# Optimization experiments

Measured on AMD Instinct MI355X. Metric: run time of the kernel, lower is better.

Reference implementation:

```python
import jax, jax.numpy as jnp
import numpy as np

TEMPERATURE = 0.04
LAMBDA_KOLEO = 0.1
EPS_NORM = 1e-12
EPS_KOLEO = 1e-9


def setup_inputs() -> dict:
    key = jax.random.key(0)
    k1, k2 = jax.random.split(key)
    N, D = 8192, 512
    z1 = jax.random.normal(k1, (N, D), dtype=jnp.float32)
    z2 = jax.random.normal(k2, (N, D), dtype=jnp.float32)
    return {"z1": z1, "z2": z2}


def _l2_normalize(x):
    # matches F.normalize(x, dim=1) with default eps=1e-12
    n = jnp.linalg.norm(x, axis=1, keepdims=True)
    return x / jnp.maximum(n, EPS_NORM)


def _infonce(queries, keys, temperature):
    # [N, N] similarity logits; labels are the diagonal
    logits = (queries @ keys.T) / temperature
    logp = jax.nn.log_softmax(logits, axis=1)
    return -jnp.mean(jnp.diagonal(logp))


def _koleo(emb):
    # pairwise euclidean distances via gram trick (matches torch.cdist p=2)
    sq = jnp.sum(emb * emb, axis=1)
    d2 = sq[:, None] + sq[None, :] - 2.0 * (emb @ emb.T)
    d = jnp.sqrt(jnp.maximum(d2, 0.0))
    N = emb.shape[0]
    eye = jnp.eye(N, dtype=bool)
    d = jnp.where(eye, jnp.inf, d)
    min_d = jnp.min(d, axis=1)
    return -jnp.mean(jnp.log(min_d + EPS_KOLEO))


def reference(z1, z2):
    z1 = _l2_normalize(z1)
    z2 = _l2_normalize(z2)
    loss_12 = _infonce(z1, z2, TEMPERATURE)
    loss_21 = _infonce(z2, z1, TEMPERATURE)
    loss_contrastive = (loss_12 + loss_21) / 2
    koleo_1 = _koleo(z1)
    koleo_2 = _koleo(z2)
    loss_koleo = (koleo_1 + koleo_2) / 2
    total_loss = loss_contrastive + LAMBDA_KOLEO * loss_koleo
    return total_loss
```

## Files before the change

kernel.cpp:

```cpp
#include <hip/hip_runtime.h>
#include <hip/hip_bf16.h>
#include <hip/hip_fp8.h>
#include <math.h>

#define N 8192
#define D 512
#define BM 128
#define BK 64
#define NSTRIP 64
#define S_BLOCKS (NSTRIP * NSTRIP)
#define TRI (NSTRIP * (NSTRIP + 1) / 2)
#define G_BLOCKS (2 * TRI)
#define SG_BLOCKS (S_BLOCKS + G_BLOCKS)

typedef float f32x16 __attribute__((ext_vector_type(16)));
typedef int i32x4 __attribute__((ext_vector_type(4)));
typedef int i32x8 __attribute__((ext_vector_type(8)));

__device__ inline void gload_lds16(const void* g, void* l) {
  __builtin_amdgcn_global_load_lds(
      (const __attribute__((address_space(1))) void*)g,
      (__attribute__((address_space(3))) void*)l, 16, 0, 0);
}

__global__ __launch_bounds__(256) void norm_kernel(
    const float* __restrict__ z1, const float* __restrict__ z2,
    unsigned char* __restrict__ q1, unsigned char* __restrict__ q2,
    float* __restrict__ diag, float* __restrict__ out) {
  int t = threadIdx.x;
  int lane = t & 63;
  int w = t >> 6;
  int row = blockIdx.x * 4 + w;
  if (blockIdx.x == 0 && t == 0) out[0] = 0.0f;
  const float4* a = (const float4*)(z1 + (size_t)row * D);
  const float4* b = (const float4*)(z2 + (size_t)row * D);
  float4 xa0 = a[lane], xa1 = a[lane + 64];
  float4 xb0 = b[lane], xb1 = b[lane + 64];
  float ss1 = xa0.x * xa0.x + xa0.y * xa0.y + xa0.z * xa0.z + xa0.w * xa0.w +
              xa1.x * xa1.x + xa1.y * xa1.y + xa1.z * xa1.z + xa1.w * xa1.w;
  float ss2 = xb0.x * xb0.x + xb0.y * xb0.y + xb0.z * xb0.z + xb0.w * xb0.w +
              xb1.x * xb1.x + xb1.y * xb1.y + xb1.z * xb1.z + xb1.w * xb1.w;
  float dd = xa0.x * xb0.x + xa0.y * xb0.y + xa0.z * xb0.z + xa0.w * xb0.w +
             xa1.x * xb1.x + xa1.y * xb1.y + xa1.z * xb1.z + xa1.w * xb1.w;
#pragma unroll
  for (int off = 1; off < 64; off <<= 1) {
    ss1 += __shfl_xor(ss1, off);
    ss2 += __shfl_xor(ss2, off);
    dd  += __shfl_xor(dd,  off);
  }
  float i1 = 1.0f / fmaxf(sqrtf(ss1), 1e-12f);
  float i2 = 1.0f / fmaxf(sqrtf(ss2), 1e-12f);
  float fa[8] = {xa0.x, xa0.y, xa0.z, xa0.w, xa1.x, xa1.y, xa1.z, xa1.w};
  float fb[8] = {xb0.x, xb0.y, xb0.z, xb0.w, xb1.x, xb1.y, xb1.z, xb1.w};
  unsigned int u1[2], u2[2];
#pragma unroll
  for (int g = 0; g < 2; g++) {
    unsigned int v1 = 0, v2 = 0;
#pragma unroll
    for (int e = 0; e < 4; e++) {
      __hip_fp8_e4m3 c1(fa[g * 4 + e] * i1);
      __hip_fp8_e4m3 c2(fb[g * 4 + e] * i2);
      v1 |= ((unsigned int)c1.__x) << (8 * e);
      v2 |= ((unsigned int)c2.__x) << (8 * e);
    }
    u1[g] = v1; u2[g] = v2;
  }
  ((unsigned int*)q1)[(size_t)row * 128 + lane] = u1[0];
  ((unsigned int*)q1)[(size_t)row * 128 + 64 + lane] = u1[1];
  ((unsigned int*)q2)[(size_t)row * 128 + lane] = u2[0];
  ((unsigned int*)q2)[(size_t)row * 128 + 64 + lane] = u2[1];
  if (lane == 0) diag[row] = dd * i1 * i2;
}

__device__ __forceinline__ void stage_pair(
    const unsigned char* pA, const unsigned char* pB,
    unsigned char (*Ab)[BM * BK], unsigned char (*Bb)[BM * BK],
    int ldst, int chunk) {
  int buf = chunk & 3;
  int k0 = chunk * BK;
  gload_lds16(pA + k0, &Ab[buf][ldst]);
  gload_lds16(pA + 64 * D + k0, &Ab[buf][4096 + ldst]);
  gload_lds16(pB + k0, &Bb[buf][ldst]);
  gload_lds16(pB + 64 * D + k0, &Bb[buf][4096 + ldst]);
}

#define SG_ROUND(p, VM)                                                        \
  {                                                                            \
    asm volatile("s_waitcnt vmcnt(" #VM ")" ::: "memory");                     \
    __builtin_amdgcn_s_barrier();                                              \
    __builtin_amdgcn_sched_barrier(0);                                         \
    if ((p) < 5) stage_pair(pA, pB, Ab, Bb, ldst, (p) + 3);                    \
    const unsigned char* Ac = Ab[(p) & 3];                                     \
    const unsigned char* Bc = Bb[(p) & 3];                                     \
    i32x8 af[2], bf[2];                                                        \
    _Pragma("unroll")                                                          \
    for (int i = 0; i < 2; i++) {                                              \
      i32x4 lo = *(const i32x4*)(Ac + offA[i][0]);                             \
      i32x4 hi = *(const i32x4*)(Ac + offA[i][1]);                             \
      af[i] = __builtin_shufflevector(lo, hi, 0, 1, 2, 3, 4, 5, 6, 7);         \
      lo = *(const i32x4*)(Bc + offB[i][0]);                                   \
      hi = *(const i32x4*)(Bc + offB[i][1]);                                   \
      bf[i] = __builtin_shufflevector(lo, hi, 0, 1, 2, 3, 4, 5, 6, 7);         \
    }                                                                          \
    asm volatile("s_waitcnt lgkmcnt(0)" ::: "memory");                         \
    __builtin_amdgcn_sched_barrier(0);                                         \
    __builtin_amdgcn_s_setprio(1);                                             \
    _Pragma("unroll")                                                          \
    for (int i = 0; i < 2; i++)                                                \
      _Pragma("unroll")                                                        \
      for (int j = 0; j < 2; j++)                                              \
        acc[i][j] = __builtin_amdgcn_mfma_scale_f32_32x32x64_f8f6f4(           \
            af[i], bf[j], acc[i][j], 0, 0, 0, 0x7F7F7F7F, 0, 0x7F7F7F7F);      \
    __builtin_amdgcn_s_setprio(0);                                             \
    __builtin_amdgcn_sched_barrier(0);                                         \
  }

__device__ __forceinline__ void mm_tile_mx(
    const unsigned char* __restrict__ X, const unsigned char* __restrict__ Y,
    int r0, int c0, unsigned char (*Ab)[BM * BK], unsigned char (*Bb)[BM * BK],
    f32x16 (&acc)[2][2], int t, int l31, int h, int rw, int cw) {
#pragma unroll
  for (int i = 0; i < 2; i++)
#pragma unroll
    for (int j = 0; j < 2; j++)
#pragma unroll
      for (int r = 0; r < 16; r++) acc[i][j][r] = 0.0f;

  int srow = t >> 2;
  int ssrc = (t & 3) ^ ((t >> 3) & 3);
  const unsigned char* pA = X + (size_t)(r0 + srow) * D + ssrc * 16;
  const unsigned char* pB = Y + (size_t)(c0 + srow) * D + ssrc * 16;
  int ldst = t * 16;

  int offA[2][2], offB[2][2];
#pragma unroll
  for (int i = 0; i < 2; i++) {
    int row = rw * 64 + i * 32 + l31;
    int sw = (row >> 1) & 3;
    offA[i][0] = row * 64 + (((h << 1) | 0) ^ sw) * 16;
    offA[i][1] = row * 64 + (((h << 1) | 1) ^ sw) * 16;
  }
#pragma unroll
  for (int j = 0; j < 2; j++) {
    int row = cw * 64 + j * 32 + l31;
    int sw = (row >> 1) & 3;
    offB[j][0] = row * 64 + (((h << 1) | 0) ^ sw) * 16;
    offB[j][1] = row * 64 + (((h << 1) | 1) ^ sw) * 16;
  }

  stage_pair(pA, pB, Ab, Bb, ldst, 0);
  stage_pair(pA, pB, Ab, Bb, ldst, 1);
  stage_pair(pA, pB, Ab, Bb, ldst, 2);

  SG_ROUND(0, 8) SG_ROUND(1, 8) SG_ROUND(2, 8) SG_ROUND(3, 8)
  SG_ROUND(4, 8) SG_ROUND(5, 8) SG_ROUND(6, 4) SG_ROUND(7, 0)
}

__global__ __launch_bounds__(256, 2) void sg_kernel(
    const unsigned char* __restrict__ q1, const unsigned char* __restrict__ q2,
    float* __restrict__ rowS, float* __restrict__ colS,
    float* __restrict__ partG) {
  __shared__ unsigned char Ab[4][BM * BK];
  __shared__ unsigned char Bb[4][BM * BK];
  float (*redA)[BM] = reinterpret_cast<float (*)[BM]>(&Ab[0][0]);
  float (*redB)[BM] = reinterpret_cast<float (*)[BM]>(&Ab[0][0] + 1024);

  int bx = blockIdx.x;
  int t = threadIdx.x;
  int lane = t & 63;
  int wave = t >> 6;
  int l31 = lane & 31;
  int h = lane >> 5;
  int rw = wave >> 1;
  int cw = wave & 1;
  const float scale = 1.4426950408889634f / 0.04f;

  bool smode = bx < S_BLOCKS;
  const unsigned char* X;
  const unsigned char* Y;
  int r0, c0, ga = 0, gb = 0, gg = 0;
  bool diagb = false;
  if (smode) {
    r0 = (bx >> 6) * BM;
    c0 = (bx & 63) * BM;
    X = q1; Y = q2;
  } else {
    int gx = bx - S_BLOCKS;
    gg = (gx >= TRI) ? 1 : 0;
    int tri = gx - gg * TRI;
    int a = (int)((sqrtf(8.0f * (float)tri + 1.0f) - 1.0f) * 0.5f);
    while ((a + 1) * (a + 2) / 2 <= tri) a++;
    while (a * (a + 1) / 2 > tri) a--;
    int b = tri - a * (a + 1) / 2;
    ga = a; gb = b;
    X = gg ? q2 : q1; Y = X;
    r0 = a * BM;
    c0 = b * BM;
    diagb = (a == b);
  }

  f32x16 acc[2][2];
  mm_tile_mx(X, Y, r0, c0, Ab, Bb, acc, t, l31, h, rw, cw);

  __syncthreads();

  if (smode) {
    float csum[2] = {0.0f, 0.0f};
#pragma unroll
    for (int i = 0; i < 2; i++) {
      float rsum[16];
#pragma unroll
      for (int reg = 0; reg < 16; reg++) rsum[reg] = 0.0f;
#pragma unroll
      for (int j = 0; j < 2; j++)
#pragma unroll
        for (int reg = 0; reg < 16; reg++) {
          float e = __builtin_amdgcn_exp2f(acc[i][j][reg] * scale);
          rsum[reg] += e;
          csum[j] += e;
        }
#pragma unroll
      for (int reg = 0; reg < 16; reg++) {
#pragma unroll
        for (int off = 1; off < 32; off <<= 1) rsum[reg] += __shfl_xor(rsum[reg], off);
      }
      if (l31 == 0) {
#pragma unroll
        for (int reg = 0; reg < 16; reg++) {
          int rloc = (reg & 3) + 8 * (reg >> 2) + 4 * h;
          redB[cw][rw * 64 + i * 32 + rloc] = rsum[reg];
        }
      }
    }
#pragma unroll
    for (int j = 0; j < 2; j++) {
      csum[j] += __shfl_xor(csum[j], 32);
      if (h == 0) redA[rw][cw * 64 + j * 32 + l31] = csum[j];
    }
    __syncthreads();
    if (t < BM) {
      colS[(size_t)(r0 >> 7) * N + c0 + t] = redA[0][t] + redA[1][t];
      rowS[(size_t)(c0 >> 7) * N + r0 + t] = redB[0][t] + redB[1][t];
    }
  } else {
#pragma unroll
    for (int i = 0; i < 2; i++) {
      float rmax[16];
#pragma unroll
      for (int reg = 0; reg < 16; reg++) {
        int rloc = (reg & 3) + 8 * (reg >> 2) + 4 * h;
        int rr = rw * 64 + i * 32 + rloc;
        float v = -3.0e38f;
#pragma unroll
        for (int j = 0; j < 2; j++) {
          float x = acc[i][j][reg];
          int cc = cw * 64 + j * 32 + l31;
          if (diagb && cc == rr) x = -3.0e38f;
          v = fmaxf(v, x);
        }
        rmax[reg] = v;
      }
#pragma unroll
      for (int reg = 0; reg < 16; reg++) {
#pragma unroll
        for (int off = 1; off < 32; off <<= 1) rmax[reg] = fmaxf(rmax[reg], __shfl_xor(rmax[reg], off));
      }
      if (l31 == 0) {
#pragma unroll
        for (int reg = 0; reg < 16; reg++) {
          int rloc = (reg & 3) + 8 * (reg >> 2) + 4 * h;
          redA[cw][rw * 64 + i * 32 + rloc] = rmax[reg];
        }
      }
    }
    if (!diagb) {
#pragma unroll
      for (int j = 0; j < 2; j++) {
        float m = -3.0e38f;
#pragma unroll
        for (int i = 0; i < 2; i++)
#pragma unroll
          for (int reg = 0; reg < 16; reg++) m = fmaxf(m, acc[i][j][reg]);
        m = fmaxf(m, __shfl_xor(m, 32));
        if (h == 0) redB[rw][cw * 64 + j * 32 + l31] = m;
      }
    }
    __syncthreads();
    if (t < BM) {
      partG[((size_t)(gg * NSTRIP + gb)) * N + r0 + t] = fmaxf(redA[0][t], redA[1][t]);
      if (!diagb)
        partG[((size_t)(gg * NSTRIP + ga)) * N + c0 + t] = fmaxf(redB[0][t], redB[1][t]);
    }
  }
}

__global__ __launch_bounds__(256) void combine_kernel(
    const float* __restrict__ diag,
    const float* __restrict__ rowS, const float* __restrict__ colS,
    const float* __restrict__ partG, float* __restrict__ out) {
  int t = threadIdx.x;
  int l = t & 63;
  int w = t >> 6;
  int i = blockIdx.x * 64 + l;

  float sR = 0.0f, sC = 0.0f, g1 = -3.0e38f, g2 = -3.0e38f;
#pragma unroll
  for (int s = 0; s < 16; s++) {
    int strip = w * 16 + s;
    sR += rowS[(size_t)strip * N + i];
    sC += colS[(size_t)strip * N + i];
    g1 = fmaxf(g1, partG[(size_t)strip * N + i]);
    g2 = fmaxf(g2, partG[(size_t)(NSTRIP + strip) * N + i]);
  }
  __shared__ float red[4][4][64];
  red[0][w][l] = sR; red[1][w][l] = sC; red[2][w][l] = g1; red[3][w][l] = g2;
  __syncthreads();
  if (w == 0) {
    sR = red[0][0][l] + red[0][1][l] + red[0][2][l] + red[0][3][l];
    sC = red[1][0][l] + red[1][1][l] + red[1][2][l] + red[1][3][l];
    g1 = fmaxf(fmaxf(red[2][0][l], red[2][1][l]), fmaxf(red[2][2][l], red[2][3][l]));
    g2 = fmaxf(fmaxf(red[3][0][l], red[3][1][l]), fmaxf(red[3][2][l], red[3][3][l]));
    float dv = diag[i] * 25.0f;
    float a12 = logf(sR) - dv;
    float a21 = logf(sC) - dv;
    float k1 = logf(sqrtf(fmaxf(2.0f - 2.0f * g1, 0.0f)) + 1e-9f);
    float k2 = logf(sqrtf(fmaxf(2.0f - 2.0f * g2, 0.0f)) + 1e-9f);
    float c = 0.5f * (a12 + a21) / (float)N - 0.1f * 0.5f * (k1 + k2) / (float)N;
#pragma unroll
    for (int off = 1; off < 64; off <<= 1) c += __shfl_xor(c, off);
    if (l == 0) atomicAdd(out, c);
  }
}

extern "C" void kernel_launch(void* const* d_in, const int* in_sizes, int n_in,
                              void* d_out, int out_size, void* d_ws, size_t ws_size,
                              hipStream_t stream) {
  const float* z1 = (const float*)d_in[0];
  const float* z2 = (const float*)d_in[1];
  char* w = (char*)d_ws;
  unsigned char* q1 = (unsigned char*)w; w += (size_t)N * D;
  unsigned char* q2 = (unsigned char*)w; w += (size_t)N * D;
  float* diag = (float*)w;   w += (size_t)N * sizeof(float);
  float* rowS = (float*)w;   w += (size_t)NSTRIP * N * sizeof(float);
  float* colS = (float*)w;   w += (size_t)NSTRIP * N * sizeof(float);
  float* partG = (float*)w;  w += (size_t)2 * NSTRIP * N * sizeof(float);
  float* out = (float*)d_out;

  norm_kernel<<<N / 4, 256, 0, stream>>>(z1, z2, q1, q2, diag, out);
  sg_kernel<<<SG_BLOCKS, 256, 0, stream>>>(q1, q2, rowS, colS, partG);
  combine_kernel<<<N / 64, 256, 0, stream>>>(diag, rowS, colS, partG, out);
}
```

Measured before the change: 233.5 us.

## Enlarge similarity GEMM tiles to 256x256 with 8 waves and XCD-aware block mapping

Doubles the output tile of the fused FP8 similarity/Gram kernel from 128 to 256 rows and columns. Each block now runs 512 threads, each wave computing a 128x64 sub-tile, with a 128KB dynamic LDS four-stage buffer. Block indices are remapped so that blocks sharing bx&7 (likely the same XCD) work on neighbouring tiles, which should improve L2 reuse. The goal is higher arithmetic intensity and fewer global loads, at the cost of more registers, more LDS, lower occupancy, and a coarser tail.

```diff
diff --git a/kernel.cpp b/kernel.cpp
--- a/kernel.cpp
+++ b/kernel.cpp
@@ -5,13 +5,13 @@
 
 #define N 8192
 #define D 512
-#define BM 128
+#define BM 256
 #define BK 64
-#define NSTRIP 64
+#define NSTRIP 32
 #define S_BLOCKS (NSTRIP * NSTRIP)
-#define TRI (NSTRIP * (NSTRIP + 1) / 2)
-#define G_BLOCKS (2 * TRI)
+#define G_BLOCKS 1056
 #define SG_BLOCKS (S_BLOCKS + G_BLOCKS)
+#define QPX 260
 
 typedef float f32x16 __attribute__((ext_vector_type(16)));
 typedef int i32x4 __attribute__((ext_vector_type(4)));
@@ -72,16 +72,15 @@
   if (lane == 0) diag[row] = dd * i1 * i2;
 }
 
-__device__ __forceinline__ void stage_pair(
+__device__ __forceinline__ void stage_chunk(
     const unsigned char* pA, const unsigned char* pB,
-    unsigned char (*Ab)[BM * BK], unsigned char (*Bb)[BM * BK],
-    int ldst, int chunk) {
-  int buf = chunk & 3;
+    unsigned char* ldsb, int t, int chunk) {
+  unsigned char* buf = ldsb + (chunk & 3) * 32768;
   int k0 = chunk * BK;
-  gload_lds16(pA + k0, &Ab[buf][ldst]);
-  gload_lds16(pA + 64 * D + k0, &Ab[buf][4096 + ldst]);
-  gload_lds16(pB + k0, &Bb[buf][ldst]);
-  gload_lds16(pB + 64 * D + k0, &Bb[buf][4096 + ldst]);
+  gload_lds16(pA + k0,           buf + t * 16);
+  gload_lds16(pA + 128 * D + k0, buf + 8192 + t * 16);
+  gload_lds16(pB + k0,           buf + 16384 + t * 16);
+  gload_lds16(pB + 128 * D + k0, buf + 24576 + t * 16);
 }
 
 #define SG_ROUND(p, VM)                                                        \
@@ -89,24 +88,26 @@
     asm volatile("s_waitcnt vmcnt(" #VM ")" ::: "memory");                     \
     __builtin_amdgcn_s_barrier();                                              \
     __builtin_amdgcn_sched_barrier(0);                                         \
-    if ((p) < 5) stage_pair(pA, pB, Ab, Bb, ldst, (p) + 3);                    \
-    const unsigned char* Ac = Ab[(p) & 3];                                     \
-    const unsigned char* Bc = Bb[(p) & 3];                                     \
-    i32x8 af[2], bf[2];                                                        \
+    if ((p) < 5) stage_chunk(pA, pB, lds, t, (p) + 3);                         \
+    const unsigned char* buf = lds + (((p) & 3) * 32768);                      \
+    i32x8 af[4], bf[2];                                                        \
     _Pragma("unroll")                                                          \
-    for (int i = 0; i < 2; i++) {                                              \
-      i32x4 lo = *(const i32x4*)(Ac + offA[i][0]);                             \
-      i32x4 hi = *(const i32x4*)(Ac + offA[i][1]);                             \
+    for (int i = 0; i < 4; i++) {                                              \
+      i32x4 lo = *(const i32x4*)(buf + offA[i][0]);                            \
+      i32x4 hi = *(const i32x4*)(buf + offA[i][1]);                            \
       af[i] = __builtin_shufflevector(lo, hi, 0, 1, 2, 3, 4, 5, 6, 7);         \
-      lo = *(const i32x4*)(Bc + offB[i][0]);                                   \
-      hi = *(const i32x4*)(Bc + offB[i][1]);                                   \
-      bf[i] = __builtin_shufflevector(lo, hi, 0, 1, 2, 3, 4, 5, 6, 7);         \
+    }                                                                          \
+    _Pragma("unroll")                                                          \
+    for (int j = 0; j < 2; j++) {                                              \
+      i32x4 lo = *(const i32x4*)(buf + 16384 + offB[j][0]);                    \
+      i32x4 hi = *(const i32x4*)(buf + 16384 + offB[j][1]);                    \
+      bf[j] = __builtin_shufflevector(lo, hi, 0, 1, 2, 3, 4, 5, 6, 7);         \
     }                                                                          \
     asm volatile("s_waitcnt lgkmcnt(0)" ::: "memory");                         \
     __builtin_amdgcn_sched_barrier(0);                                         \
     __builtin_amdgcn_s_setprio(1);                                             \
     _Pragma("unroll")                                                          \
-    for (int i = 0; i < 2; i++)                                                \
+    for (int i = 0; i < 4; i++)                                                \
       _Pragma("unroll")                                                        \
       for (int j = 0; j < 2; j++)                                              \
         acc[i][j] = __builtin_amdgcn_mfma_scale_f32_32x32x64_f8f6f4(           \
@@ -115,27 +116,71 @@
     __builtin_amdgcn_sched_barrier(0);                                         \
   }
 
-__device__ __forceinline__ void mm_tile_mx(
-    const unsigned char* __restrict__ X, const unsigned char* __restrict__ Y,
-    int r0, int c0, unsigned char (*Ab)[BM * BK], unsigned char (*Bb)[BM * BK],
-    f32x16 (&acc)[2][2], int t, int l31, int h, int rw, int cw) {
-#pragma unroll
-  for (int i = 0; i < 2; i++)
-#pragma unroll
-    for (int j = 0; j < 2; j++)
-#pragma unroll
-      for (int r = 0; r < 16; r++) acc[i][j][r] = 0.0f;
-
-  int srow = t >> 2;
-  int ssrc = (t & 3) ^ ((t >> 3) & 3);
-  const unsigned char* pA = X + (size_t)(r0 + srow) * D + ssrc * 16;
-  const unsigned char* pB = Y + (size_t)(c0 + srow) * D + ssrc * 16;
-  int ldst = t * 16;
-
-  int offA[2][2], offB[2][2];
-#pragma unroll
-  for (int i = 0; i < 2; i++) {
-    int row = rw * 64 + i * 32 + l31;
+__global__ __launch_bounds__(512, 2) void sg_kernel(
+    const unsigned char* __restrict__ q1, const unsigned char* __restrict__ q2,
+    float* __restrict__ rowS, float* __restrict__ colS,
+    float* __restrict__ partG) {
+  extern __shared__ unsigned char lds[];
+  float (*redR)[256] = (float (*)[256])lds;
+  float (*redC)[256] = (float (*)[256])(lds + 4096);
+
+  int bx = blockIdx.x;
+  int x = bx & 7;
+  int q = bx >> 3;
+  int t = threadIdx.x;
+  int lane = t & 63;
+  int wv = t >> 6;
+  int l31 = lane & 31;
+  int h = lane >> 5;
+  int rw = wv >> 2;
+  int cw = wv & 3;
+  const float scale = 1.4426950408889634f / 0.04f;
+
+  bool smode = q < 128;
+  const unsigned char* X;
+  const unsigned char* Y;
+  int r0, c0, ga = 0, gb = 0, gg = 0;
+  bool diagb = false;
+  if (smode) {
+    int u = x >> 1, v = x & 1;
+    int r = u * 8 + (q >> 4);
+    int c = v * 16 + (q & 15);
+    r0 = r * BM; c0 = c * BM;
+    X = q1; Y = q2;
+  } else {
+    int qq = q - 128;
+    int a4, b4, g;
+    if (qq < 20) {
+      g = qq / 10;
+      int tt = qq - g * 10;
+      int da = (int)((sqrtf(8.0f * (float)tt + 1.0f) - 1.0f) * 0.5f);
+      while ((da + 1) * (da + 2) / 2 <= tt) da++;
+      while (da * (da + 1) / 2 > tt) da--;
+      int db = tt - da * (da + 1) / 2;
+      a4 = x * 4 + da; b4 = x * 4 + db;
+    } else {
+      int e = qq - 20;
+      int n = e >> 4;
+      int tt = e & 15;
+      int pidx = x + 8 * n;
+      g = (pidx >= 28) ? 1 : 0;
+      int p = pidx - g * 28;
+      int i = (int)((sqrtf(8.0f * (float)p + 1.0f) + 1.0f) * 0.5f);
+      while (i * (i - 1) / 2 > p) i--;
+      while ((i + 1) * i / 2 <= p) i++;
+      int j = p - i * (i - 1) / 2;
+      a4 = i * 4 + (tt >> 2); b4 = j * 4 + (tt & 3);
+    }
+    ga = a4; gb = b4; gg = g;
+    X = g ? q2 : q1; Y = X;
+    r0 = a4 * BM; c0 = b4 * BM;
+    diagb = (a4 == b4);
+  }
+
+  int offA[4][2], offB[2][2];
+#pragma unroll
+  for (int i = 0; i < 4; i++) {
+    int row = rw * 128 + i * 32 + l31;
     int sw = (row >> 1) & 3;
     offA[i][0] = row * 64 + (((h << 1) | 0) ^ sw) * 16;
     offA[i][1] = row * 64 + (((h << 1) | 1) ^ sw) * 16;
@@ -148,128 +193,95 @@
     offB[j][1] = row * 64 + (((h << 1) | 1) ^ sw) * 16;
   }
 
-  stage_pair(pA, pB, Ab, Bb, ldst, 0);
-  stage_pair(pA, pB, Ab, Bb, ldst, 1);
-  stage_pair(pA, pB, Ab, Bb, ldst, 2);
+  int srow = t >> 2;
+  int ssrc = (t & 3) ^ ((t >> 3) & 3);
+  const unsigned char* pA = X + (size_t)(r0 + srow) * D + ssrc * 16;
+  const unsigned char* pB = Y + (size_t)(c0 + srow) * D + ssrc * 16;
+
+  f32x16 acc[4][2];
+#pragma unroll
+  for (int i = 0; i < 4; i++)
+#pragma unroll
+    for (int j = 0; j < 2; j++)
+#pragma unroll
+      for (int r = 0; r < 16; r++) acc[i][j][r] = 0.0f;
+
+  stage_chunk(pA, pB, lds, t, 0);
+  stage_chunk(pA, pB, lds, t, 1);
+  stage_chunk(pA, pB, lds, t, 2);
 
   SG_ROUND(0, 8) SG_ROUND(1, 8) SG_ROUND(2, 8) SG_ROUND(3, 8)
   SG_ROUND(4, 8) SG_ROUND(5, 8) SG_ROUND(6, 4) SG_ROUND(7, 0)
-}
-
-__global__ __launch_bounds__(256, 2) void sg_kernel(
-    const unsigned char* __restrict__ q1, const unsigned char* __restrict__ q2,
-    float* __restrict__ rowS, float* __restrict__ colS,
-    float* __restrict__ partG) {
-  __shared__ unsigned char Ab[4][BM * BK];
-  __shared__ unsigned char Bb[4][BM * BK];
-  float (*redA)[BM] = reinterpret_cast<float (*)[BM]>(&Ab[0][0]);
-  float (*redB)[BM] = reinterpret_cast<float (*)[BM]>(&Ab[0][0] + 1024);
-
-  int bx = blockIdx.x;
-  int t = threadIdx.x;
-  int lane = t & 63;
-  int wave = t >> 6;
-  int l31 = lane & 31;
-  int h = lane >> 5;
-  int rw = wave >> 1;
-  int cw = wave & 1;
-  const float scale = 1.4426950408889634f / 0.04f;
-
-  bool smode = bx < S_BLOCKS;
-  const unsigned char* X;
-  const unsigned char* Y;
-  int r0, c0, ga = 0, gb = 0, gg = 0;
-  bool diagb = false;
-  if (smode) {
-    r0 = (bx >> 6) * BM;
-    c0 = (bx & 63) * BM;
-    X = q1; Y = q2;
-  } else {
-    int gx = bx - S_BLOCKS;
-    gg = (gx >= TRI) ? 1 : 0;
-    int tri = gx - gg * TRI;
-    int a = (int)((sqrtf(8.0f * (float)tri + 1.0f) - 1.0f) * 0.5f);
-    while ((a + 1) * (a + 2) / 2 <= tri) a++;
-    while (a * (a + 1) / 2 > tri) a--;
-    int b = tri - a * (a + 1) / 2;
-    ga = a; gb = b;
-    X = gg ? q2 : q1; Y = X;
-    r0 = a * BM;
-    c0 = b * BM;
-    diagb = (a == b);
-  }
-
-  f32x16 acc[2][2];
-  mm_tile_mx(X, Y, r0, c0, Ab, Bb, acc, t, l31, h, rw, cw);
 
   __syncthreads();
 
   if (smode) {
     float csum[2] = {0.0f, 0.0f};
 #pragma unroll
-    for (int i = 0; i < 2; i++) {
+    for (int i = 0; i < 4; i++) {
       float rsum[16];
 #pragma unroll
-      for (int reg = 0; reg < 16; reg++) rsum[reg] = 0.0f;
+      for (int r = 0; r < 16; r++) rsum[r] = 0.0f;
 #pragma unroll
       for (int j = 0; j < 2; j++)
 #pragma unroll
-        for (int reg = 0; reg < 16; reg++) {
-          float e = __builtin_amdgcn_exp2f(acc[i][j][reg] * scale);
-          rsum[reg] += e;
+        for (int r = 0; r < 16; r++) {
+          float e = __builtin_amdgcn_exp2f(acc[i][j][r] * scale);
+          rsum[r] += e;
           csum[j] += e;
         }
 #pragma unroll
-      for (int reg = 0; reg < 16; reg++) {
-#pragma unroll
-        for (int off = 1; off < 32; off <<= 1) rsum[reg] += __shfl_xor(rsum[reg], off);
+      for (int r = 0; r < 16; r++) {
+#pragma unroll
+        for (int off = 1; off < 32; off <<= 1) rsum[r] += __shfl_xor(rsum[r], off);
       }
       if (l31 == 0) {
 #pragma unroll
-        for (int reg = 0; reg < 16; reg++) {
-          int rloc = (reg & 3) + 8 * (reg >> 2) + 4 * h;
-          redB[cw][rw * 64 + i * 32 + rloc] = rsum[reg];
+        for (int r = 0; r < 16; r++) {
+          int rloc = (r & 3) + 8 * (r >> 2) + 4 * h;
+          redR[cw][rw * 128 + i * 32 + rloc] = rsum[r];
         }
       }
     }
 #pragma unroll
     for (int j = 0; j < 2; j++) {
       csum[j] += __shfl_xor(csum[j], 32);
-      if (h == 0) redA[rw][cw * 64 + j * 32 + l31] = csum[j];
+      if (h == 0) redC[rw][cw * 64 + j * 32 + l31] = csum[j];
     }
     __syncthreads();
     if (t < BM) {
-      colS[(size_t)(r0 >> 7) * N + c0 + t] = redA[0][t] + redA[1][t];
-      rowS[(size_t)(c0 >> 7) * N + r0 + t] = redB[0][t] + redB[1][t];
+      rowS[(size_t)(c0 >> 8) * N + r0 + t] =
+          redR[0][t] + redR[1][t] + redR[2][t] + redR[3][t];
+      colS[(size_t)(r0 >> 8) * N + c0 + t] = redC[0][t] + redC[1][t];
     }
   } else {
 #pragma unroll
-    for (int i = 0; i < 2; i++) {
+    for (int i = 0; i < 4; i++) {
       float rmax[16];
 #pragma unroll
-      for (int reg = 0; reg < 16; reg++) {
-        int rloc = (reg & 3) + 8 * (reg >> 2) + 4 * h;
-        int rr = rw * 64 + i * 32 + rloc;
+      for (int r = 0; r < 16; r++) {
+        int rloc = (r & 3) + 8 * (r >> 2) + 4 * h;
+        int rr = rw * 128 + i * 32 + rloc;
         float v = -3.0e38f;
 #pragma unroll
         for (int j = 0; j < 2; j++) {
-          float x = acc[i][j][reg];
+          float xv = acc[i][j][r];
           int cc = cw * 64 + j * 32 + l31;
-          if (diagb && cc == rr) x = -3.0e38f;
-          v = fmaxf(v, x);
+          if (diagb && cc == rr) xv = -3.0e38f;
+          v = fmaxf(v, xv);
         }
-        rmax[reg] = v;
-      }
-#pragma unroll
-      for (int reg = 0; reg < 16; reg++) {
-#pragma unroll
-        for (int off = 1; off < 32; off <<= 1) rmax[reg] = fmaxf(rmax[reg], __shfl_xor(rmax[reg], off));
+        rmax[r] = v;
+      }
+#pragma unroll
+      for (int r = 0; r < 16; r++) {
+#pragma unroll
+        for (int off = 1; off < 32; off <<= 1) rmax[r] = fmaxf(rmax[r], __shfl_xor(rmax[r], off));
       }
       if (l31 == 0) {
 #pragma unroll
-        for (int reg = 0; reg < 16; reg++) {
-          int rloc = (reg & 3) + 8 * (reg >> 2) + 4 * h;
-          redA[cw][rw * 64 + i * 32 + rloc] = rmax[reg];
+        for (int r = 0; r < 16; r++) {
+          int rloc = (r & 3) + 8 * (r >> 2) + 4 * h;
+          redR[cw][rw * 128 + i * 32 + rloc] = rmax[r];
         }
       }
     }
@@ -278,18 +290,19 @@
       for (int j = 0; j < 2; j++) {
         float m = -3.0e38f;
 #pragma unroll
-        for (int i = 0; i < 2; i++)
-#pragma unroll
-          for (int reg = 0; reg < 16; reg++) m = fmaxf(m, acc[i][j][reg]);
+        for (int i = 0; i < 4; i++)
+#pragma unroll
+          for (int r = 0; r < 16; r++) m = fmaxf(m, acc[i][j][r]);
         m = fmaxf(m, __shfl_xor(m, 32));
-        if (h == 0) redB[rw][cw * 64 + j * 32 + l31] = m;
+        if (h == 0) redC[rw][cw * 64 + j * 32 + l31] = m;
       }
     }
     __syncthreads();
     if (t < BM) {
-      partG[((size_t)(gg * NSTRIP + gb)) * N + r0 + t] = fmaxf(redA[0][t], redA[1][t]);
+      partG[((size_t)(gg * NSTRIP + gb)) * N + r0 + t] =
+          fmaxf(fmaxf(redR[0][t], redR[1][t]), fmaxf(redR[2][t], redR[3][t]));
       if (!diagb)
-        partG[((size_t)(gg * NSTRIP + ga)) * N + c0 + t] = fmaxf(redB[0][t], redB[1][t]);
+        partG[((size_t)(gg * NSTRIP + ga)) * N + c0 + t] = fmaxf(redC[0][t], redC[1][t]);
     }
   }
 }
@@ -305,8 +318,8 @@
 
   float sR = 0.0f, sC = 0.0f, g1 = -3.0e38f, g2 = -3.0e38f;
 #pragma unroll
-  for (int s = 0; s < 16; s++) {
-    int strip = w * 16 + s;
+  for (int s = 0; s < 8; s++) {
+    int strip = w * 8 + s;
     sR += rowS[(size_t)strip * N + i];
     sC += colS[(size_t)strip * N + i];
     g1 = fmaxf(g1, partG[(size_t)strip * N + i]);
@@ -346,7 +359,14 @@
   float* partG = (float*)w;  w += (size_t)2 * NSTRIP * N * sizeof(float);
   float* out = (float*)d_out;
 
+  static bool attr_done = false;
+  if (!attr_done) {
+    hipFuncSetAttribute((const void*)sg_kernel,
+                        hipFuncAttributeMaxDynamicSharedMemorySize, 131072);
+    attr_done = true;
+  }
+
   norm_kernel<<<N / 4, 256, 0, stream>>>(z1, z2, q1, q2, diag, out);
-  sg_kernel<<<SG_BLOCKS, 256, 0, stream>>>(q1, q2, rowS, colS, partG);
+  sg_kernel<<<SG_BLOCKS, 512, 131072, stream>>>(q1, q2, rowS, colS, partG);
   combine_kernel<<<N / 64, 256, 0, stream>>>(diag, rowS, colS, partG, out);
 }
```

Measured after the change: 222.9 us. 4.6% less time.

## Shrink LDS pipeline to double buffer and raise occupancy to four blocks

Applied to the files above, without the earlier changes.

The GEMM tile pipeline goes from four LDS stages holding three chunks in flight to two stages holding one chunk of prefetch. This cuts shared memory per block from 64KB to 32KB so launch bounds can ask for four blocks per CU. The LDS swizzle is also reworked into a single offset per fragment, with the high half read via XOR 16 and a row-group bit added to the staging source. The trade is shallower prefetch and a full vmcnt(0) wait each round, with more waves per CU expected to hide latency in its place.

```diff
diff --git a/kernel.cpp b/kernel.cpp
--- a/kernel.cpp
+++ b/kernel.cpp
@@ -72,34 +72,32 @@
   if (lane == 0) diag[row] = dd * i1 * i2;
 }
 
-__device__ __forceinline__ void stage_pair(
+__device__ __forceinline__ void stage_chunk(
     const unsigned char* pA, const unsigned char* pB,
-    unsigned char (*Ab)[BM * BK], unsigned char (*Bb)[BM * BK],
-    int ldst, int chunk) {
-  int buf = chunk & 3;
+    unsigned char (*lds)[16384], int t, int chunk) {
+  unsigned char* buf = lds[chunk & 1];
   int k0 = chunk * BK;
-  gload_lds16(pA + k0, &Ab[buf][ldst]);
-  gload_lds16(pA + 64 * D + k0, &Ab[buf][4096 + ldst]);
-  gload_lds16(pB + k0, &Bb[buf][ldst]);
-  gload_lds16(pB + 64 * D + k0, &Bb[buf][4096 + ldst]);
-}
-
-#define SG_ROUND(p, VM)                                                        \
+  gload_lds16(pA + k0,          buf + t * 16);
+  gload_lds16(pA + 64 * D + k0, buf + 4096 + t * 16);
+  gload_lds16(pB + k0,          buf + 8192 + t * 16);
+  gload_lds16(pB + 64 * D + k0, buf + 12288 + t * 16);
+}
+
+#define SG_ROUND(p)                                                            \
   {                                                                            \
-    asm volatile("s_waitcnt vmcnt(" #VM ")" ::: "memory");                     \
+    asm volatile("s_waitcnt vmcnt(0)" ::: "memory");                           \
     __builtin_amdgcn_s_barrier();                                              \
     __builtin_amdgcn_sched_barrier(0);                                         \
-    if ((p) < 5) stage_pair(pA, pB, Ab, Bb, ldst, (p) + 3);                    \
-    const unsigned char* Ac = Ab[(p) & 3];                                     \
-    const unsigned char* Bc = Bb[(p) & 3];                                     \
+    if ((p) < 7) stage_chunk(pA, pB, lds, t, (p) + 1);                         \
+    const unsigned char* buf = lds[(p) & 1];                                   \
     i32x8 af[2], bf[2];                                                        \
     _Pragma("unroll")                                                          \
     for (int i = 0; i < 2; i++) {                                              \
-      i32x4 lo = *(const i32x4*)(Ac + offA[i][0]);                             \
-      i32x4 hi = *(const i32x4*)(Ac + offA[i][1]);                             \
+      i32x4 lo = *(const i32x4*)(buf + offA[i]);                               \
+      i32x4 hi = *(const i32x4*)(buf + (offA[i] ^ 16));                        \
       af[i] = __builtin_shufflevector(lo, hi, 0, 1, 2, 3, 4, 5, 6, 7);         \
-      lo = *(const i32x4*)(Bc + offB[i][0]);                                   \
-      hi = *(const i32x4*)(Bc + offB[i][1]);                                   \
+      lo = *(const i32x4*)(buf + offB[i]);                                     \
+      hi = *(const i32x4*)(buf + (offB[i] ^ 16));                              \
       bf[i] = __builtin_shufflevector(lo, hi, 0, 1, 2, 3, 4, 5, 6, 7);         \
     }                                                                          \
     asm volatile("s_waitcnt lgkmcnt(0)" ::: "memory");                         \
@@ -115,55 +113,13 @@
     __builtin_amdgcn_sched_barrier(0);                                         \
   }
 
-__device__ __forceinline__ void mm_tile_mx(
-    const unsigned char* __restrict__ X, const unsigned char* __restrict__ Y,
-    int r0, int c0, unsigned char (*Ab)[BM * BK], unsigned char (*Bb)[BM * BK],
-    f32x16 (&acc)[2][2], int t, int l31, int h, int rw, int cw) {
-#pragma unroll
-  for (int i = 0; i < 2; i++)
-#pragma unroll
-    for (int j = 0; j < 2; j++)
-#pragma unroll
-      for (int r = 0; r < 16; r++) acc[i][j][r] = 0.0f;
-
-  int srow = t >> 2;
-  int ssrc = (t & 3) ^ ((t >> 3) & 3);
-  const unsigned char* pA = X + (size_t)(r0 + srow) * D + ssrc * 16;
-  const unsigned char* pB = Y + (size_t)(c0 + srow) * D + ssrc * 16;
-  int ldst = t * 16;
-
-  int offA[2][2], offB[2][2];
-#pragma unroll
-  for (int i = 0; i < 2; i++) {
-    int row = rw * 64 + i * 32 + l31;
-    int sw = (row >> 1) & 3;
-    offA[i][0] = row * 64 + (((h << 1) | 0) ^ sw) * 16;
-    offA[i][1] = row * 64 + (((h << 1) | 1) ^ sw) * 16;
-  }
-#pragma unroll
-  for (int j = 0; j < 2; j++) {
-    int row = cw * 64 + j * 32 + l31;
-    int sw = (row >> 1) & 3;
-    offB[j][0] = row * 64 + (((h << 1) | 0) ^ sw) * 16;
-    offB[j][1] = row * 64 + (((h << 1) | 1) ^ sw) * 16;
-  }
-
-  stage_pair(pA, pB, Ab, Bb, ldst, 0);
-  stage_pair(pA, pB, Ab, Bb, ldst, 1);
-  stage_pair(pA, pB, Ab, Bb, ldst, 2);
-
-  SG_ROUND(0, 8) SG_ROUND(1, 8) SG_ROUND(2, 8) SG_ROUND(3, 8)
-  SG_ROUND(4, 8) SG_ROUND(5, 8) SG_ROUND(6, 4) SG_ROUND(7, 0)
-}
-
-__global__ __launch_bounds__(256, 2) void sg_kernel(
+__global__ __launch_bounds__(256, 4) void sg_kernel(
     const unsigned char* __restrict__ q1, const unsigned char* __restrict__ q2,
     float* __restrict__ rowS, float* __restrict__ colS,
     float* __restrict__ partG) {
-  __shared__ unsigned char Ab[4][BM * BK];
-  __shared__ unsigned char Bb[4][BM * BK];
-  float (*redA)[BM] = reinterpret_cast<float (*)[BM]>(&Ab[0][0]);
-  float (*redB)[BM] = reinterpret_cast<float (*)[BM]>(&Ab[0][0] + 1024);
+  __shared__ unsigned char lds[2][16384];
+  float (*redA)[BM] = reinterpret_cast<float (*)[BM]>(&lds[0][0]);
+  float (*redB)[BM] = reinterpret_cast<float (*)[BM]>(&lds[0][0] + 1024);
 
   int bx = blockIdx.x;
   int t = threadIdx.x;
@@ -199,8 +155,35 @@
     diagb = (a == b);
   }
 
+  int u = (l31 >> 4) & 1;
+  int f = (l31 >> 1) & 3;
+  int cs0 = (h << 1) ^ u ^ f;
+  int offA[2], offB[2];
+#pragma unroll
+  for (int i = 0; i < 2; i++) {
+    int rowa = rw * 64 + i * 32 + l31;
+    offA[i] = rowa * 64 + cs0 * 16;
+    int rowb = cw * 64 + i * 32 + l31;
+    offB[i] = 8192 + rowb * 64 + cs0 * 16;
+  }
+
+  int srow = t >> 2;
+  int ssrc = (t & 3) ^ ((t >> 3) & 3) ^ ((t >> 6) & 1);
+  const unsigned char* pA = X + (size_t)(r0 + srow) * D + ssrc * 16;
+  const unsigned char* pB = Y + (size_t)(c0 + srow) * D + ssrc * 16;
+
   f32x16 acc[2][2];
-  mm_tile_mx(X, Y, r0, c0, Ab, Bb, acc, t, l31, h, rw, cw);
+#pragma unroll
+  for (int i = 0; i < 2; i++)
+#pragma unroll
+    for (int j = 0; j < 2; j++)
+#pragma unroll
+      for (int r = 0; r < 16; r++) acc[i][j][r] = 0.0f;
+
+  stage_chunk(pA, pB, lds, t, 0);
+
+  SG_ROUND(0) SG_ROUND(1) SG_ROUND(2) SG_ROUND(3)
+  SG_ROUND(4) SG_ROUND(5) SG_ROUND(6) SG_ROUND(7)
 
   __syncthreads();
 
```

Result: faster. 199.9 us (-14.4%).
